# Kernel optimization log

Measured on AMD Instinct MI355X. Metric: run time of the kernel, lower is better.

## Reference

```python
import jax, jax.numpy as jnp
import numpy as np
from jax import lax


def conv3x3(x, w):
    # x: (B,C,H,W), w: (O,I,3,3); stride 1, padding 1, no bias
    return lax.conv_general_dilated(x, w, (1, 1), 'SAME',
                                    dimension_numbers=('NCHW', 'OIHW', 'NCHW'))


def group_norm(x, w, b, groups=32, eps=1e-5):
    B, C, H, W = x.shape
    xg = x.reshape(B, groups, C // groups, H, W)
    mu = xg.mean(axis=(2, 3, 4), keepdims=True)
    var = xg.var(axis=(2, 3, 4), keepdims=True)
    xg = (xg - mu) * lax.rsqrt(var + eps)
    return xg.reshape(B, C, H, W) * w[None, :, None, None] + b[None, :, None, None]


def to_patches(x, p1, p2):
    # 'b c (h p1) (w p2) -> (b h w) c (p1 p2)'
    B, C, H, W = x.shape
    h, w = H // p1, W // p2
    x = x.reshape(B, C, h, p1, w, p2).transpose(0, 2, 4, 1, 3, 5)
    return x.reshape(B * h * w, C, p1 * p2)


def from_patches(x, B, h, w, p1, p2):
    # '(b h w) c (p1 p2) -> b c (h p1) (w p2)'
    C = x.shape[1]
    x = x.reshape(B, h, w, C, p1, p2).transpose(0, 3, 1, 4, 2, 5)
    return x.reshape(B, C, h * p1, w * p2)


def setup_inputs() -> dict:
    key = jax.random.key(0)
    ks = jax.random.split(key, 5)
    B, C, H, W = 8, 256, 128, 128
    inter = 256
    s = 0.05  # keep conv outputs in a sane range
    return {
        'x_low': jax.random.normal(ks[0], (B, C, H, W), jnp.float32),
        'x_high': jax.random.normal(ks[1], (B, C, H, W), jnp.float32),
        'w_q': jax.random.normal(ks[2], (inter, C, 3, 3), jnp.float32) * s,
        'gq_w': jnp.ones((inter,), jnp.float32),
        'gq_b': jnp.zeros((inter,), jnp.float32),
        'w_k': jax.random.normal(ks[3], (inter, C, 3, 3), jnp.float32) * s,
        'gk_w': jnp.ones((inter,), jnp.float32),
        'gk_b': jnp.zeros((inter,), jnp.float32),
        'w_o': jax.random.normal(ks[4], (C, inter, 3, 3), jnp.float32) * s,
        'go_w': jnp.ones((C,), jnp.float32),
        'go_b': jnp.zeros((C,), jnp.float32),
        'p1': 8,
        'p2': 8,
    }


def reference(x_low, x_high, w_q, gq_w, gq_b, w_k, gk_w, gk_b, w_o, go_w, go_b, p1, p2):
    B, C, H, W = x_low.shape
    inter = w_q.shape[0]
    h, w = H // p1, W // p2
    # q, k: (B*h*w, inter, T) with T = p1*p2
    q = to_patches(group_norm(conv3x3(x_low, w_q), gq_w, gq_b), p1, p2)
    k = to_patches(group_norm(conv3x3(x_high, w_k), gk_w, gk_b), p1, p2)
    q = q.transpose(0, 2, 1)                                  # (N, T, inter)
    attn = jnp.matmul(q, k) / jnp.sqrt(jnp.float32(inter))    # (N, T, T)
    attn = jax.nn.softmax(attn, axis=-1)
    out = jnp.matmul(attn, k.transpose(0, 2, 1))              # (N, T, inter)
    out = from_patches(out.transpose(0, 2, 1), B, h, w, p1, p2)
    return group_norm(conv3x3(out + x_low, w_o), go_w, go_b)
```

## Files before the change

### kernel.cpp

```cpp
#include <hip/hip_runtime.h>

using u16 = unsigned short;
using u32 = unsigned int;

typedef short bfrag8 __attribute__((ext_vector_type(8)));
typedef float f32x4  __attribute__((ext_vector_type(4)));

__device__ __forceinline__ void unpack8(const int4 v, float f[8]) {
  u32 a = (u32)v.x, b = (u32)v.y, c = (u32)v.z, d = (u32)v.w;
  f[0] = __uint_as_float(a << 16);
  f[1] = __uint_as_float(a & 0xffff0000u);
  f[2] = __uint_as_float(b << 16);
  f[3] = __uint_as_float(b & 0xffff0000u);
  f[4] = __uint_as_float(c << 16);
  f[5] = __uint_as_float(c & 0xffff0000u);
  f[6] = __uint_as_float(d << 16);
  f[7] = __uint_as_float(d & 0xffff0000u);
}

__device__ __forceinline__ u16 f2bf(float f) {
  u32 u = __float_as_uint(f);
  u32 r = u + 0x7fffu + ((u >> 16) & 1u);
  return (u16)(r >> 16);
}

__device__ __forceinline__ void gload_lds16(const void* g, void* l) {
  __builtin_amdgcn_global_load_lds(
      (const __attribute__((address_space(1))) void*)g,
      (__attribute__((address_space(3))) void*)l, 16, 0, 0);
}

__global__ __launch_bounds__(256) void wprep(
    const float* __restrict__ wq, const float* __restrict__ wk, const float* __restrict__ wo,
    u16* __restrict__ dq, u16* __restrict__ dk, u16* __restrict__ dwo)
{
  const float* s = (blockIdx.y == 0) ? wq : (blockIdx.y == 1) ? wk : wo;
  u16* d = (blockIdx.y == 0) ? dq : (blockIdx.y == 1) ? dk : dwo;
  int id = blockIdx.x * 256 + threadIdx.x;
  int e = id * 4;
  int tap = e >> 16;
  int rem = e & 65535;
  int oc = rem >> 8, ic = rem & 255;
  u16 o[4];
#pragma unroll
  for (int j = 0; j < 4; ++j)
    o[j] = f2bf(s[((size_t)oc * 256 + ic + j) * 9 + tap]);
  *reinterpret_cast<uint2*>(d + e) = *reinterpret_cast<uint2*>(o);
}

__global__ __launch_bounds__(256) void xpose(
    const float* __restrict__ xa, const float* __restrict__ xb,
    u16* __restrict__ oa, u16* __restrict__ ob)
{
  const int row = blockIdx.x, b = blockIdx.y;
  const float* src = blockIdx.z ? xb : xa;
  u16* dst = blockIdx.z ? ob : oa;
  const int t = threadIdx.x;
  const int px4 = (t >> 3) * 4;
  const int c8 = (t & 7) * 8;
#pragma unroll
  for (int p = 0; p < 4; ++p) {
    int c0 = p * 64 + c8;
    float4 v[8];
#pragma unroll
    for (int j = 0; j < 8; ++j)
      v[j] = *reinterpret_cast<const float4*>(src + ((size_t)b * 256 + c0 + j) * 16384 + row * 128 + px4);
#pragma unroll
    for (int e = 0; e < 4; ++e) {
      u16 o[8];
      o[0] = f2bf(e==0?v[0].x:e==1?v[0].y:e==2?v[0].z:v[0].w);
      o[1] = f2bf(e==0?v[1].x:e==1?v[1].y:e==2?v[1].z:v[1].w);
      o[2] = f2bf(e==0?v[2].x:e==1?v[2].y:e==2?v[2].z:v[2].w);
      o[3] = f2bf(e==0?v[3].x:e==1?v[3].y:e==2?v[3].z:v[3].w);
      o[4] = f2bf(e==0?v[4].x:e==1?v[4].y:e==2?v[4].z:v[4].w);
      o[5] = f2bf(e==0?v[5].x:e==1?v[5].y:e==2?v[5].z:v[5].w);
      o[6] = f2bf(e==0?v[6].x:e==1?v[6].y:e==2?v[6].z:v[6].w);
      o[7] = f2bf(e==0?v[7].x:e==1?v[7].y:e==2?v[7].z:v[7].w);
      *reinterpret_cast<int4*>(dst + (((size_t)b * 128 + row) * 128 + px4 + e) * 256 + c0) =
          *reinterpret_cast<int4*>(o);
    }
  }
}

__global__ __launch_bounds__(256, 3) void conv_mfma(
    const u16* __restrict__ X, const u16* __restrict__ W2, u16* __restrict__ Y,
    float* __restrict__ part)
{
  __shared__ __attribute__((aligned(16))) char csm[49920];

  const int t = threadIdx.x;
  const int l = t & 63;
  const int wv = t >> 6;
  const int id = blockIdx.x;
  const int u = (id & 7) * 256 + (id >> 3);
  const int bb = u >> 8;
  const int y0 = (u >> 1) & 127;
  const int ocblk = u & 1;
  const int oc0 = ocblk * 128;
  const int och = wv >> 1, pxh = wv & 1;
  const int lc = l & 15, lq = l >> 4;
  const int sa = (lc >> 1) & 3;

  f32x4 acc[4][4];
#pragma unroll
  for (int m = 0; m < 4; ++m)
#pragma unroll
    for (int n = 0; n < 4; ++n) acc[m][n] = (f32x4){0.f, 0.f, 0.f, 0.f};

  const size_t xplane = (size_t)bb * (128 * 128 * 256);

  {
    int4 z = {0, 0, 0, 0};
    if (t < 24) {
      int q = t & 3, sel = (t >> 2) & 1, kh = t >> 3;
      int cidx = sel ? 129 : 0;
      *reinterpret_cast<int4*>(csm + ((kh * 132 + cidx) * 4 + q) * 16) = z;
    }
    if (y0 == 0)
      for (int s = t; s < 528; s += 256) *reinterpret_cast<int4*>(csm + s * 16) = z;
    if (y0 == 127)
      for (int s = t; s < 528; s += 256) *reinterpret_cast<int4*>(csm + 16896 + s * 16) = z;
  }

  auto stageA = [&](int tap, int buf, int ic0) {
#pragma unroll
    for (int i = 0; i < 2; ++i) {
      int idx = t + i * 256;
      int oc = idx >> 2, q = idx & 3;
      int qs = q ^ ((oc >> 1) & 3);
      const u16* src = W2 + (((size_t)(tap * 256 + oc0 + oc)) << 8) + ic0 + qs * 8;
      gload_lds16(src, csm + 25344 + buf * 8192 + (i * 256 + (t & ~63)) * 16);
    }
  };
  auto stageB = [&](int ic0) {
#pragma unroll
    for (int i = 0; i < 6; ++i) {
      int idx = t + i * 256;
      int kh = idx >> 9;
      int row = y0 - 1 + kh;
      if (row >= 0 && row < 128) {
        int px = (idx & 511) >> 2, q = idx & 3;
        int qs = q ^ (((px + 1) >> 1) & 3);
        const u16* src = X + xplane + (((size_t)(row * 128 + px)) << 8) + ic0 + qs * 8;
        gload_lds16(src, csm + 64 + kh * 256 + (i * 256 + (t & ~63)) * 16);
      }
    }
  };

  bfrag8 af0[4], xf0[4], af1[4], xf1[4];

#define READF(TAP, AF, XF)                                                    \
  {                                                                           \
    const int kh_ = (TAP) / 3, kw_ = (TAP) % 3, buf_ = (TAP) % 3;             \
    const int sb_ = ((lc + kw_) >> 1) & 3;                                    \
    _Pragma("unroll")                                                         \
    for (int m = 0; m < 4; ++m)                                               \
      AF[m] = *reinterpret_cast<const bfrag8*>(csm + 25344 + buf_ * 8192 +    \
                  ((och * 64 + m * 16 + lc) * 4 + (lq ^ sa)) * 16);           \
    _Pragma("unroll")                                                         \
    for (int n = 0; n < 4; ++n) {                                             \
      int S_ = pxh * 64 + n * 16 + lc + kw_;                                  \
      XF[n] = *reinterpret_cast<const bfrag8*>(csm + kh_ * 8448 + S_ * 64 +   \
                  (lq ^ sb_) * 16);                                           \
    }                                                                         \
  }

#define DOMFMA(AF, XF)                                                        \
  {                                                                           \
    _Pragma("unroll")                                                         \
    for (int m = 0; m < 4; ++m)                                               \
      _Pragma("unroll")                                                       \
      for (int n = 0; n < 4; ++n)                                             \
        acc[m][n] = __builtin_amdgcn_mfma_f32_16x16x32_bf16(AF[m], XF[n],     \
                                                            acc[m][n], 0, 0, 0); \
  }

  stageB(0);
  stageA(0, 0, 0);
  stageA(1, 1, 0);
  __syncthreads();

  for (int chunk = 0; chunk < 8; ++chunk) {
    const int ic0 = chunk * 32;
    READF(0, af0, xf0);
#pragma unroll
    for (int tap = 0; tap < 9; ++tap) {
      asm volatile("s_waitcnt lgkmcnt(0)" ::: "memory");
      __builtin_amdgcn_sched_barrier(0);
      if (tap <= 6) stageA(tap + 2, (tap + 2) % 3, ic0);
      if (tap <= 6) {
        asm volatile("s_waitcnt vmcnt(2)" ::: "memory");
      } else if (tap == 7) {
        asm volatile("s_waitcnt vmcnt(0)" ::: "memory");
      }
      __builtin_amdgcn_sched_barrier(0);
      __builtin_amdgcn_s_barrier();
      __builtin_amdgcn_sched_barrier(0);

      if (tap < 8) {
        if (tap & 1) { READF(tap + 1, af0, xf0); }
        else         { READF(tap + 1, af1, xf1); }
      }
      __builtin_amdgcn_s_setprio(1);
      if (tap & 1) { DOMFMA(af1, xf1); }
      else         { DOMFMA(af0, xf0); }
      __builtin_amdgcn_s_setprio(0);
    }
    if (chunk < 7) {
      stageA(0, 0, ic0 + 32);
      stageA(1, 1, ic0 + 32);
      stageB(ic0 + 32);
      __syncthreads();
    }
  }
#undef READF
#undef DOMFMA

  u16* Ost = (u16*)csm;
  float* sst = (float*)(csm + 34816);
  const int chb = och * 64 + lq * 4;
  const int pxb = pxh * 64 + lc;
  __syncthreads();
#pragma unroll
  for (int m = 0; m < 4; ++m)
#pragma unroll
    for (int n = 0; n < 4; ++n) {
      u32 lo = (u32)f2bf(acc[m][n][0]) | ((u32)f2bf(acc[m][n][1]) << 16);
      u32 hi = (u32)f2bf(acc[m][n][2]) | ((u32)f2bf(acc[m][n][3]) << 16);
      uint2 pk = {lo, hi};
      *reinterpret_cast<uint2*>(&Ost[(pxb + n * 16) * 136 + chb + m * 16]) = pk;
    }
#pragma unroll
  for (int m = 0; m < 4; ++m)
#pragma unroll
    for (int r = 0; r < 4; ++r) {
      float s  = acc[m][0][r] + acc[m][1][r] + acc[m][2][r] + acc[m][3][r];
      float ss = acc[m][0][r] * acc[m][0][r] + acc[m][1][r] * acc[m][1][r] +
                 acc[m][2][r] * acc[m][2][r] + acc[m][3][r] * acc[m][3][r];
#pragma unroll
      for (int off = 1; off < 16; off <<= 1) {
        s  += __shfl_xor(s, off);
        ss += __shfl_xor(ss, off);
      }
      if (lc == 0) {
        int c = och * 64 + m * 16 + lq * 4 + r;
        sst[pxh * 256 + c]       = s;
        sst[pxh * 256 + 128 + c] = ss;
      }
    }
  __syncthreads();

  if (t < 128) {
    float s  = sst[t]       + sst[256 + t];
    float ss = sst[128 + t] + sst[384 + t];
    size_t pb = (((size_t)bb * 128 + y0) * 256 + oc0 + t) * 2;
    part[pb]     = s;
    part[pb + 1] = ss;
  }
#pragma unroll
  for (int s8 = 0; s8 < 8; ++s8) {
    int pix = s8 * 16 + (t >> 4);
    int sub = t & 15;
    int4 v = *reinterpret_cast<const int4*>(&Ost[pix * 136 + sub * 8]);
    *reinterpret_cast<int4*>(Y + xplane + (((size_t)(y0 * 128 + pix)) << 8) + oc0 + sub * 8) = v;
  }
}

__global__ __launch_bounds__(256) void gnstat2b(const float* __restrict__ part, float* __restrict__ stat)
{
  const int b = blockIdx.x, t = threadIdx.x;
  float s = 0.f, ss = 0.f;
  for (int row = 0; row < 128; ++row) {
    size_t pb = (((size_t)b * 128 + row) * 256 + t) * 2;
    s  += part[pb];
    ss += part[pb + 1];
  }
  __shared__ float Ls[256], Lss[256];
  Ls[t] = s; Lss[t] = ss;
  __syncthreads();
  if (t < 32) {
    float S = 0.f, SS = 0.f;
#pragma unroll
    for (int j = 0; j < 8; ++j) { S += Ls[t * 8 + j]; SS += Lss[t * 8 + j]; }
    float mean = S * (1.f / 131072.f);
    float var = SS * (1.f / 131072.f) - mean * mean;
    stat[b * 32 + t] = mean;
    stat[256 + b * 32 + t] = rsqrtf(var + 1e-5f);
  }
}

__global__ __launch_bounds__(256) void normkT(
    const u16* __restrict__ yk, const float* __restrict__ statk,
    const float* __restrict__ gkw, const float* __restrict__ gkb,
    u16* __restrict__ kT)
{
  __shared__ u16 L[8][264];
  const int y = blockIdx.x, b = blockIdx.y;
  const int ph = y >> 3, py = y & 7;
  const int t = threadIdx.x;
  const int px = t >> 5, c8 = (t & 31) * 8;
  const int g = c8 >> 3;
  float mean = statk[b * 32 + g], rstd = statk[256 + b * 32 + g];
  float A[8], Bv[8];
#pragma unroll
  for (int j = 0; j < 8; ++j) {
    A[j] = rstd * gkw[c8 + j];
    Bv[j] = gkb[c8 + j] - mean * A[j];
  }
  const size_t rowbase = (((size_t)b * 128 + y) * 128) * 256;
  const size_t outbase = ((size_t)(b * 16 + ph) * 8 + py) * 32768;
  for (int pw = 0; pw < 16; ++pw) {
    int4 v = *reinterpret_cast<const int4*>(yk + rowbase + (size_t)(pw * 8 + px) * 256 + c8);
    float f[8]; unpack8(v, f);
    u16 o[8];
#pragma unroll
    for (int j = 0; j < 8; ++j) o[j] = f2bf(f[j] * A[j] + Bv[j]);
    *reinterpret_cast<int4*>(&L[px][c8]) = *reinterpret_cast<int4*>(o);
    __syncthreads();
    u16 o2[8];
#pragma unroll
    for (int q = 0; q < 8; ++q) o2[q] = L[q][t];
    *reinterpret_cast<int4*>(kT + outbase + (size_t)(pw * 256 + t) * 8) = *reinterpret_cast<int4*>(o2);
    __syncthreads();
  }
}

#define OST 280
__global__ __launch_bounds__(256, 3) void attn_mfma(
    const u16* __restrict__ yq, const u16* __restrict__ yk,
    const u16* __restrict__ kT, const u16* __restrict__ xl,
    const float* __restrict__ statq, const float* __restrict__ statk,
    const float* __restrict__ gqw, const float* __restrict__ gqb,
    const float* __restrict__ gkw,
    u16* __restrict__ resid)
{
  __shared__ __attribute__((aligned(16))) u16 smem[64 * OST + 4 * 16 * 72];
  u16* Ost = smem;
  u16* Pls = smem + 64 * OST;

  const int n = blockIdx.x;
  const int b = n >> 8, ph = (n >> 4) & 15, pw = n & 15;
  const int t = threadIdx.x, l = t & 63, w = t >> 6;
  const int lc = l & 15, lg = l >> 4;

  auto tokaddr = [&](int tok) -> size_t {
    return (((size_t)(b * 128 + ph * 8 + (tok >> 3))) * 128 + pw * 8 + (tok & 7)) * 256;
  };

  const size_t qa = tokaddr(16 * w + lc) + lg * 8;
  bfrag8 aF[8];
#pragma unroll
  for (int ks = 0; ks < 8; ++ks) {
    int c0 = lg * 8 + ks * 32;
    int g = ks * 4 + lg;
    float meanq = statq[b * 32 + g], rstdq = statq[256 + b * 32 + g];
    float rstdk = statk[256 + b * 32 + g];
    int4 v = *reinterpret_cast<const int4*>(yq + qa + ks * 32);
    float f[8]; unpack8(v, f);
    float4 w0 = *reinterpret_cast<const float4*>(gqw + c0);
    float4 w1 = *reinterpret_cast<const float4*>(gqw + c0 + 4);
    float4 b0 = *reinterpret_cast<const float4*>(gqb + c0);
    float4 b1 = *reinterpret_cast<const float4*>(gqb + c0 + 4);
    float4 k0 = *reinterpret_cast<const float4*>(gkw + c0);
    float4 k1 = *reinterpret_cast<const float4*>(gkw + c0 + 4);
    float ww[8] = {w0.x, w0.y, w0.z, w0.w, w1.x, w1.y, w1.z, w1.w};
    float bb[8] = {b0.x, b0.y, b0.z, b0.w, b1.x, b1.y, b1.z, b1.w};
    float kk[8] = {k0.x, k0.y, k0.z, k0.w, k1.x, k1.y, k1.z, k1.w};
    u16 o[8];
#pragma unroll
    for (int j = 0; j < 8; ++j) {
      float Aq = rstdq * ww[j];
      float Bq = bb[j] - meanq * Aq;
      float Ak = rstdk * kk[j];
      o[j] = f2bf((f[j] * Aq + Bq) * Ak);
    }
    aF[ks] = *reinterpret_cast<bfrag8*>(o);
  }

  f32x4 sacc[4];
#pragma unroll
  for (int nt = 0; nt < 4; ++nt) sacc[nt] = (f32x4){0.f, 0.f, 0.f, 0.f};

#pragma unroll
  for (int nt = 0; nt < 4; ++nt) {
    const size_t ka = tokaddr(nt * 16 + lc) + lg * 8;
    bfrag8 bF[8];
#pragma unroll
    for (int ks = 0; ks < 8; ++ks)
      bF[ks] = *reinterpret_cast<const bfrag8*>(yk + ka + ks * 32);
#pragma unroll
    for (int ks = 0; ks < 8; ++ks)
      sacc[nt] = __builtin_amdgcn_mfma_f32_16x16x32_bf16(aF[ks], bF[ks], sacc[nt], 0, 0, 0);
  }

  u16* Pw = Pls + w * (16 * 72);
#pragma unroll
  for (int r = 0; r < 4; ++r) {
    float m0 = fmaxf(fmaxf(sacc[0][r], sacc[1][r]), fmaxf(sacc[2][r], sacc[3][r]));
    m0 = fmaxf(m0, __shfl_xor(m0, 1));
    m0 = fmaxf(m0, __shfl_xor(m0, 2));
    m0 = fmaxf(m0, __shfl_xor(m0, 4));
    m0 = fmaxf(m0, __shfl_xor(m0, 8));
    float p0 = __expf((sacc[0][r] - m0) * 0.0625f);
    float p1 = __expf((sacc[1][r] - m0) * 0.0625f);
    float p2 = __expf((sacc[2][r] - m0) * 0.0625f);
    float p3 = __expf((sacc[3][r] - m0) * 0.0625f);
    float s0 = p0 + p1 + p2 + p3;
    s0 += __shfl_xor(s0, 1);
    s0 += __shfl_xor(s0, 2);
    s0 += __shfl_xor(s0, 4);
    s0 += __shfl_xor(s0, 8);
    float inv = 1.f / s0;
    int prow = (lg * 4 + r) * 72;
    Pw[prow + 0 * 16 + lc] = f2bf(p0 * inv);
    Pw[prow + 1 * 16 + lc] = f2bf(p1 * inv);
    Pw[prow + 2 * 16 + lc] = f2bf(p2 * inv);
    Pw[prow + 3 * 16 + lc] = f2bf(p3 * inv);
  }

  bfrag8 pA[2];
#pragma unroll
  for (int js = 0; js < 2; ++js)
    pA[js] = *reinterpret_cast<const bfrag8*>(Pw + lc * 72 + js * 32 + lg * 8);

  f32x4 pacc[16];
#pragma unroll
  for (int ct = 0; ct < 16; ++ct) pacc[ct] = (f32x4){0.f, 0.f, 0.f, 0.f};

#pragma unroll
  for (int ct = 0; ct < 16; ++ct) {
    bfrag8 vB[2];
#pragma unroll
    for (int js = 0; js < 2; ++js)
      vB[js] = *reinterpret_cast<const bfrag8*>(
          kT + ((size_t)((b * 16 + ph) * 8 + js * 4 + lg)) * 32768 +
          (size_t)(pw * 256 + ct * 16 + lc) * 8);
#pragma unroll
    for (int js = 0; js < 2; ++js)
      pacc[ct] = __builtin_amdgcn_mfma_f32_16x16x32_bf16(pA[js], vB[js], pacc[ct], 0, 0, 0);
  }

#pragma unroll
  for (int ct = 0; ct < 16; ++ct)
#pragma unroll
    for (int r = 0; r < 4; ++r)
      Ost[(16 * w + lg * 4 + r) * OST + ct * 16 + lc] = f2bf(pacc[ct][r]);
  __syncthreads();

#pragma unroll
  for (int s = 0; s < 8; ++s) {
    int px_ = t >> 5;
    int c16 = t & 31;
    size_t g = (((size_t)b * 128 + ph * 8 + s) * 128 + pw * 8 + px_) * 256 + c16 * 8;
    int4 o = *reinterpret_cast<const int4*>(&Ost[(s * 8 + px_) * OST + c16 * 8]);
    int4 r = *reinterpret_cast<const int4*>(xl + g);
    float fo[8], fr[8]; unpack8(o, fo); unpack8(r, fr);
    u16 pk[8];
#pragma unroll
    for (int j = 0; j < 8; ++j) pk[j] = f2bf(fo[j] + fr[j]);
    *reinterpret_cast<int4*>(resid + g) = *reinterpret_cast<int4*>(pk);
  }
}

__global__ __launch_bounds__(256) void gnapply_t(
    const u16* __restrict__ Y, const float* __restrict__ stat,
    const float* __restrict__ gw, const float* __restrict__ gb,
    float* __restrict__ out)
{
  const int row = blockIdx.x, b = blockIdx.y;
  const int t = threadIdx.x;
  const int px4 = (t & 31) * 4;
  const int c8 = (t >> 5) * 8;
#pragma unroll
  for (int p = 0; p < 4; ++p) {
    int c0 = p * 64 + c8;
    int g = c0 >> 3;
    float mean = stat[b * 32 + g], rstd = stat[256 + b * 32 + g];
    float A[8], Bv[8];
#pragma unroll
    for (int j = 0; j < 8; ++j) {
      A[j] = rstd * gw[c0 + j];
      Bv[j] = gb[c0 + j] - mean * A[j];
    }
    float vals[4][8];
#pragma unroll
    for (int e = 0; e < 4; ++e) {
      int4 v = *reinterpret_cast<const int4*>(Y + (((size_t)b * 128 + row) * 128 + px4 + e) * 256 + c0);
      float f[8]; unpack8(v, f);
#pragma unroll
      for (int j = 0; j < 8; ++j) vals[e][j] = fmaf(f[j], A[j], Bv[j]);
    }
#pragma unroll
    for (int j = 0; j < 8; ++j) {
      float4 o = {vals[0][j], vals[1][j], vals[2][j], vals[3][j]};
      *reinterpret_cast<float4*>(out + ((size_t)b * 256 + c0 + j) * 16384 + row * 128 + px4) = o;
    }
  }
}

extern "C" void kernel_launch(void* const* d_in, const int* in_sizes, int n_in,
                              void* d_out, int out_size, void* d_ws, size_t ws_size,
                              hipStream_t stream)
{
  const float* x_low  = (const float*)d_in[0];
  const float* x_high = (const float*)d_in[1];
  const float* w_q    = (const float*)d_in[2];
  const float* gq_w   = (const float*)d_in[3];
  const float* gq_b   = (const float*)d_in[4];
  const float* w_k    = (const float*)d_in[5];
  const float* gk_w   = (const float*)d_in[6];
  const float* gk_b   = (const float*)d_in[7];
  const float* w_o    = (const float*)d_in[8];
  const float* go_w   = (const float*)d_in[9];
  const float* go_b   = (const float*)d_in[10];
  float* out = (float*)d_out;

  char* ws = (char*)d_ws;
  const size_t slot = 67108864;
  u16* xl  = (u16*)(ws + 0 * slot);
  u16* xh  = (u16*)(ws + 1 * slot);
  u16* yq  = (u16*)(ws + 2 * slot);
  u16* yk  = (u16*)(ws + 3 * slot);
  u16* kT  = (u16*)(ws + 4 * slot);
  u16* W2q = (u16*)(ws + 5 * slot);
  u16* W2k = W2q + 589824;
  u16* W2o = W2k + 589824;
  float* partq = (float*)(ws + 5 * slot + 3 * 1179648);
  float* partk = partq + 524288;
  float* parto = partk + 524288;
  float* statq = parto + 524288;
  float* statk = statq + 512;
  float* stato = statk + 512;

  wprep<<<dim3(576, 3), 256, 0, stream>>>(w_q, w_k, w_o, W2q, W2k, W2o);
  xpose<<<dim3(128, 8, 2), 256, 0, stream>>>(x_low, x_high, xl, xh);
  conv_mfma<<<2048, 256, 0, stream>>>(xl, W2q, yq, partq);
  conv_mfma<<<2048, 256, 0, stream>>>(xh, W2k, yk, partk);
  gnstat2b<<<8, 256, 0, stream>>>(partq, statq);
  gnstat2b<<<8, 256, 0, stream>>>(partk, statk);
  normkT<<<dim3(128, 8), 256, 0, stream>>>(yk, statk, gk_w, gk_b, kT);
  attn_mfma<<<2048, 256, 0, stream>>>(yq, yk, kT, xl, statq, statk,
                                      gq_w, gq_b, gk_w, xh);
  conv_mfma<<<2048, 256, 0, stream>>>(xh, W2o, xl, parto);
  gnstat2b<<<8, 256, 0, stream>>>(parto, stato);
  gnapply_t<<<dim3(128, 8), 256, 0, stream>>>(xl, stato, go_w, go_b, out);
}
```

Measured before the change: 696.3 us.

## Pipeline input-plane staging across channel chunks in conv GEMM loop

```diff
diff --git a/kernel.cpp b/kernel.cpp
--- a/kernel.cpp
+++ b/kernel.cpp
@@ -132,30 +132,29 @@
       gload_lds16(src, csm + 25344 + buf * 8192 + (i * 256 + (t & ~63)) * 16);
     }
   };
-  auto stageB = [&](int ic0) {
-#pragma unroll
-    for (int i = 0; i < 6; ++i) {
-      int idx = t + i * 256;
-      int kh = idx >> 9;
-      int row = y0 - 1 + kh;
-      if (row >= 0 && row < 128) {
-        int px = (idx & 511) >> 2, q = idx & 3;
+  auto stageBplane = [&](int p, int ic0) {
+    int row = y0 - 1 + p;
+    if (row >= 0 && row < 128) {
+#pragma unroll
+      for (int i = 0; i < 2; ++i) {
+        int idx = t + i * 256;
+        int px = idx >> 2, q = idx & 3;
         int qs = q ^ (((px + 1) >> 1) & 3);
         const u16* src = X + xplane + (((size_t)(row * 128 + px)) << 8) + ic0 + qs * 8;
-        gload_lds16(src, csm + 64 + kh * 256 + (i * 256 + (t & ~63)) * 16);
+        gload_lds16(src, csm + p * 8448 + 64 + (i * 256 + (t & ~63)) * 16);
       }
     }
   };
 
   bfrag8 af0[4], xf0[4], af1[4], xf1[4];
 
-#define READF(TAP, AF, XF)                                                    \
+#define READF(NT9, BUF, AF, XF)                                               \
   {                                                                           \
-    const int kh_ = (TAP) / 3, kw_ = (TAP) % 3, buf_ = (TAP) % 3;             \
+    const int kh_ = (NT9) / 3, kw_ = (NT9) % 3;                               \
     const int sb_ = ((lc + kw_) >> 1) & 3;                                    \
     _Pragma("unroll")                                                         \
     for (int m = 0; m < 4; ++m)                                               \
-      AF[m] = *reinterpret_cast<const bfrag8*>(csm + 25344 + buf_ * 8192 +    \
+      AF[m] = *reinterpret_cast<const bfrag8*>(csm + 25344 + (BUF) * 8192 +   \
                   ((och * 64 + m * 16 + lc) * 4 + (lq ^ sa)) * 16);           \
     _Pragma("unroll")                                                         \
     for (int n = 0; n < 4; ++n) {                                             \
@@ -175,42 +174,54 @@
                                                             acc[m][n], 0, 0, 0); \
   }
 
-  stageB(0);
+  stageBplane(0, 0);
+  stageBplane(1, 0);
+  stageBplane(2, 0);
   stageA(0, 0, 0);
   stageA(1, 1, 0);
   __syncthreads();
-
-  for (int chunk = 0; chunk < 8; ++chunk) {
-    const int ic0 = chunk * 32;
-    READF(0, af0, xf0);
-#pragma unroll
-    for (int tap = 0; tap < 9; ++tap) {
+  READF(0, 0, af0, xf0);
+
+  for (int c2 = 0; c2 < 4; ++c2) {
+    const int icb = c2 * 64;
+#pragma unroll
+    for (int t18 = 0; t18 < 18; ++t18) {
       asm volatile("s_waitcnt lgkmcnt(0)" ::: "memory");
       __builtin_amdgcn_sched_barrier(0);
-      if (tap <= 6) stageA(tap + 2, (tap + 2) % 3, ic0);
-      if (tap <= 6) {
-        asm volatile("s_waitcnt vmcnt(2)" ::: "memory");
-      } else if (tap == 7) {
-        asm volatile("s_waitcnt vmcnt(0)" ::: "memory");
+
+      bool bIn = false;
+      if (t18 == 0)       { if (c2 >= 1) { stageBplane(2, icb);      bIn = (y0 != 127); } }
+      else if (t18 == 3)  { stageBplane(0, icb + 32);                bIn = (y0 != 0); }
+      else if (t18 == 6)  { stageBplane(1, icb + 32);                bIn = true; }
+      else if (t18 == 9)  { stageBplane(2, icb + 32);                bIn = (y0 != 127); }
+      else if (t18 == 12) { if (c2 < 3) { stageBplane(0, icb + 64);  bIn = (y0 != 0); } }
+      else if (t18 == 15) { if (c2 < 3) { stageBplane(1, icb + 64);  bIn = true; } }
+
+      const bool aStaged = !(c2 == 3 && t18 >= 16);
+      if (aStaged) {
+        const int tapA = (t18 + 2) % 9;
+        const int icA  = (c2 * 2 + (t18 + 2) / 9) * 32;
+        stageA(tapA, (t18 + 2) % 3, icA);
       }
-      __builtin_amdgcn_sched_barrier(0);
-      __builtin_amdgcn_s_barrier();
-      __builtin_amdgcn_sched_barrier(0);
-
-      if (tap < 8) {
-        if (tap & 1) { READF(tap + 1, af0, xf0); }
-        else         { READF(tap + 1, af1, xf1); }
+
+      if (!(c2 == 3 && t18 == 17)) {
+        const int n = (aStaged ? 2 : 0) + (bIn ? 2 : 0);
+        if (n == 4)      { asm volatile("s_waitcnt vmcnt(4)" ::: "memory"); }
+        else if (n == 2) { asm volatile("s_waitcnt vmcnt(2)" ::: "memory"); }
+        else             { asm volatile("s_waitcnt vmcnt(0)" ::: "memory"); }
+        __builtin_amdgcn_sched_barrier(0);
+        __builtin_amdgcn_s_barrier();
+        __builtin_amdgcn_sched_barrier(0);
+        const int nt9 = (t18 + 1) % 9;
+        const int nbuf = (t18 + 1) % 3;
+        if (t18 & 1) { READF(nt9, nbuf, af0, xf0); }
+        else         { READF(nt9, nbuf, af1, xf1); }
       }
+
       __builtin_amdgcn_s_setprio(1);
-      if (tap & 1) { DOMFMA(af1, xf1); }
+      if (t18 & 1) { DOMFMA(af1, xf1); }
       else         { DOMFMA(af0, xf0); }
       __builtin_amdgcn_s_setprio(0);
-    }
-    if (chunk < 7) {
-      stageA(0, 0, ic0 + 32);
-      stageA(1, 1, ic0 + 32);
-      stageB(ic0 + 32);
-      __syncthreads();
     }
   }
 #undef READF
@@ -325,7 +336,7 @@
   }
 }
 
-#define OST 280
+#define OST 272
 __global__ __launch_bounds__(256, 3) void attn_mfma(
     const u16* __restrict__ yq, const u16* __restrict__ yk,
     const u16* __restrict__ kT, const u16* __restrict__ xl,
```

After: 1.041 ms. 1.5x slower.

## Fuse K transpose into conv epilogue and defer K GroupNorm past softmax-V

Applied to the files above, without the earlier changes.

```diff
diff --git a/kernel.cpp b/kernel.cpp
--- a/kernel.cpp
+++ b/kernel.cpp
@@ -84,7 +84,7 @@
 
 __global__ __launch_bounds__(256, 3) void conv_mfma(
     const u16* __restrict__ X, const u16* __restrict__ W2, u16* __restrict__ Y,
-    float* __restrict__ part)
+    float* __restrict__ part, u16* __restrict__ kTout)
 {
   __shared__ __attribute__((aligned(16))) char csm[49920];
 
@@ -264,6 +264,21 @@
     int4 v = *reinterpret_cast<const int4*>(&Ost[pix * 136 + sub * 8]);
     *reinterpret_cast<int4*>(Y + xplane + (((size_t)(y0 * 128 + pix)) << 8) + oc0 + sub * 8) = v;
   }
+
+  if (kTout) {
+    const size_t outbase = ((size_t)(bb * 16 + (y0 >> 3)) * 8 + (y0 & 7)) * 32768;
+    const int half = t >> 7;
+    const int cl = t & 127;
+#pragma unroll
+    for (int i = 0; i < 8; ++i) {
+      int pw = i * 2 + half;
+      u16 o[8];
+#pragma unroll
+      for (int j = 0; j < 8; ++j) o[j] = Ost[(pw * 8 + j) * 136 + cl];
+      *reinterpret_cast<int4*>(kTout + outbase + (size_t)(pw * 256 + oc0 + cl) * 8) =
+          *reinterpret_cast<int4*>(o);
+    }
+  }
 }
 
 __global__ __launch_bounds__(256) void gnstat2b(const float* __restrict__ part, float* __restrict__ stat)
@@ -289,49 +304,13 @@
   }
 }
 
-__global__ __launch_bounds__(256) void normkT(
-    const u16* __restrict__ yk, const float* __restrict__ statk,
-    const float* __restrict__ gkw, const float* __restrict__ gkb,
-    u16* __restrict__ kT)
-{
-  __shared__ u16 L[8][264];
-  const int y = blockIdx.x, b = blockIdx.y;
-  const int ph = y >> 3, py = y & 7;
-  const int t = threadIdx.x;
-  const int px = t >> 5, c8 = (t & 31) * 8;
-  const int g = c8 >> 3;
-  float mean = statk[b * 32 + g], rstd = statk[256 + b * 32 + g];
-  float A[8], Bv[8];
-#pragma unroll
-  for (int j = 0; j < 8; ++j) {
-    A[j] = rstd * gkw[c8 + j];
-    Bv[j] = gkb[c8 + j] - mean * A[j];
-  }
-  const size_t rowbase = (((size_t)b * 128 + y) * 128) * 256;
-  const size_t outbase = ((size_t)(b * 16 + ph) * 8 + py) * 32768;
-  for (int pw = 0; pw < 16; ++pw) {
-    int4 v = *reinterpret_cast<const int4*>(yk + rowbase + (size_t)(pw * 8 + px) * 256 + c8);
-    float f[8]; unpack8(v, f);
-    u16 o[8];
-#pragma unroll
-    for (int j = 0; j < 8; ++j) o[j] = f2bf(f[j] * A[j] + Bv[j]);
-    *reinterpret_cast<int4*>(&L[px][c8]) = *reinterpret_cast<int4*>(o);
-    __syncthreads();
-    u16 o2[8];
-#pragma unroll
-    for (int q = 0; q < 8; ++q) o2[q] = L[q][t];
-    *reinterpret_cast<int4*>(kT + outbase + (size_t)(pw * 256 + t) * 8) = *reinterpret_cast<int4*>(o2);
-    __syncthreads();
-  }
-}
-
-#define OST 280
+#define OST 272
 __global__ __launch_bounds__(256, 3) void attn_mfma(
     const u16* __restrict__ yq, const u16* __restrict__ yk,
     const u16* __restrict__ kT, const u16* __restrict__ xl,
     const float* __restrict__ statq, const float* __restrict__ statk,
     const float* __restrict__ gqw, const float* __restrict__ gqb,
-    const float* __restrict__ gkw,
+    const float* __restrict__ gkw, const float* __restrict__ gkb,
     u16* __restrict__ resid)
 {
   __shared__ __attribute__((aligned(16))) u16 smem[64 * OST + 4 * 16 * 72];
@@ -441,10 +420,16 @@
   }
 
 #pragma unroll
-  for (int ct = 0; ct < 16; ++ct)
+  for (int ct = 0; ct < 16; ++ct) {
+    int c = ct * 16 + lc;
+    int g = c >> 3;
+    float mean = statk[b * 32 + g], rstd = statk[256 + b * 32 + g];
+    float A = rstd * gkw[c];
+    float Bv = gkb[c] - mean * A;
 #pragma unroll
     for (int r = 0; r < 4; ++r)
-      Ost[(16 * w + lg * 4 + r) * OST + ct * 16 + lc] = f2bf(pacc[ct][r]);
+      Ost[(16 * w + lg * 4 + r) * OST + ct * 16 + lc] = f2bf(fmaf(pacc[ct][r], A, Bv));
+  }
   __syncthreads();
 
 #pragma unroll
@@ -534,14 +519,13 @@
 
   wprep<<<dim3(576, 3), 256, 0, stream>>>(w_q, w_k, w_o, W2q, W2k, W2o);
   xpose<<<dim3(128, 8, 2), 256, 0, stream>>>(x_low, x_high, xl, xh);
-  conv_mfma<<<2048, 256, 0, stream>>>(xl, W2q, yq, partq);
-  conv_mfma<<<2048, 256, 0, stream>>>(xh, W2k, yk, partk);
+  conv_mfma<<<2048, 256, 0, stream>>>(xl, W2q, yq, partq, nullptr);
+  conv_mfma<<<2048, 256, 0, stream>>>(xh, W2k, yk, partk, kT);
   gnstat2b<<<8, 256, 0, stream>>>(partq, statq);
   gnstat2b<<<8, 256, 0, stream>>>(partk, statk);
-  normkT<<<dim3(128, 8), 256, 0, stream>>>(yk, statk, gk_w, gk_b, kT);
   attn_mfma<<<2048, 256, 0, stream>>>(yq, yk, kT, xl, statq, statk,
-                                      gq_w, gq_b, gk_w, xh);
-  conv_mfma<<<2048, 256, 0, stream>>>(xh, W2o, xl, parto);
+                                      gq_w, gq_b, gk_w, gk_b, xh);
+  conv_mfma<<<2048, 256, 0, stream>>>(xh, W2o, xl, parto, nullptr);
   gnstat2b<<<8, 256, 0, stream>>>(parto, stato);
   gnapply_t<<<dim3(128, 8), 256, 0, stream>>>(xl, stato, go_w, go_b, out);
 }
```

Measured after the change: 686.0 us. No clear change (-1.5%).
